# Kernel tuning notes

Hardware: AMD Instinct MI355X
Metric: run time of the kernel (lower is better)

## Reference

```python
import jax, jax.numpy as jnp
import numpy as np

H = 1024          # hidden_size
M = 512           # moe_intermediate_size
E = 16            # num_routed_experts
TOP_K = 2         # num_experts_per_tok
SCALE = 2.5       # routed_scaling_factor
NORM_TOPK = True  # norm_topk_prob
B, S = 1, 1024


def setup_inputs() -> dict:
    key = jax.random.key(0)
    ks = jax.random.split(key, 8)
    std = 0.02
    return {
        "hidden_states": jax.random.normal(ks[0], (B, S, H), jnp.float32),
        "gate_w": jax.random.normal(ks[1], (E, H), jnp.float32) * std,
        "w_gate": jax.random.normal(ks[2], (E, H, M), jnp.float32) * std,
        "w_up": jax.random.normal(ks[3], (E, H, M), jnp.float32) * std,
        "w_down": jax.random.normal(ks[4], (E, M, H), jnp.float32) * std,
        "ws_gate": jax.random.normal(ks[5], (H, M), jnp.float32) * std,
        "ws_up": jax.random.normal(ks[6], (H, M), jnp.float32) * std,
        "ws_down": jax.random.normal(ks[7], (M, H), jnp.float32) * std,
    }


def _moe(x, gate_w, w_gate, w_up, w_down, ws_gate, ws_up, ws_down):
    # x: [T, H] flattened tokens
    T = x.shape[0]
    # shared expert (SwiGLU): down(silu(gate(x)) * up(x))
    shared = (jax.nn.silu(x @ ws_gate) * (x @ ws_up)) @ ws_down  # [T, H]

    # sigmoid gating in fp32 (matches F.linear on fp32 + sigmoid)
    scores = jax.nn.sigmoid(x.astype(jnp.float32) @ gate_w.T.astype(jnp.float32))  # [T, E]
    topk_w, topk_idx = jax.lax.top_k(scores, TOP_K)  # [T, K]
    if NORM_TOPK and TOP_K > 1:
        topk_w = topk_w / (topk_w.sum(-1, keepdims=True) + 1e-20)
    topk_w = topk_w * SCALE

    # dense combine weights [T, E]; zero for non-selected experts, so weighting
    # all-expert outputs is mathematically identical to the dispatch/gather path
    route = jnp.zeros((T, E), topk_w.dtype).at[jnp.arange(T)[:, None], topk_idx].set(topk_w)

    # per-expert SwiGLU over all tokens (grouped-GEMM reference)
    g = jnp.einsum("th,ehm->etm", x, w_gate)                 # [E, T, M]
    u = jnp.einsum("th,ehm->etm", x, w_up)                   # [E, T, M]
    eo = jnp.einsum("etm,emh->eth", jax.nn.silu(g) * u, w_down)  # [E, T, H]
    routed = jnp.einsum("te,eth->th", route.astype(x.dtype), eo)  # [T, H]
    return routed + shared


def reference(hidden_states, gate_w, w_gate, w_up, w_down, ws_gate, ws_up, ws_down):
    b, s, h = hidden_states.shape
    x = hidden_states.reshape(-1, h)
    out = _moe(x, gate_w, w_gate, w_up, w_down, ws_gate, ws_up, ws_down)
    return out.reshape(b, s, h)
```

## Files before the change

### kernel.cpp

```cpp
#include <hip/hip_runtime.h>
#include <math.h>

#define TT 1024
#define HH 1024
#define MM 512
#define NE 16

typedef _Float16 f16;
typedef _Float16 f16x4 __attribute__((ext_vector_type(4)));
typedef _Float16 f16x8 __attribute__((ext_vector_type(8)));
typedef float f32x4 __attribute__((ext_vector_type(4)));

#define GLL(g, l) __builtin_amdgcn_global_load_lds(                         \
    (const __attribute__((address_space(1))) void*)(g),                     \
    (__attribute__((address_space(3))) void*)(l), 16, 0, 0)
#define SB() __builtin_amdgcn_sched_barrier(0)
#define WAITVM(N) { SB(); asm volatile("s_waitcnt vmcnt(" #N ")"); SB(); }
#define BARRIER() __builtin_amdgcn_s_barrier()

__global__ __launch_bounds__(256) void pack_k(const float* __restrict__ x, f16* __restrict__ xh)
{
    const int i = (blockIdx.x * 256 + threadIdx.x) * 4;
    float4 v = *(const float4*)(x + i);
    f16x4 h = { (f16)v.x, (f16)v.y, (f16)v.z, (f16)v.w };
    *(f16x4*)(xh + i) = h;
}

__global__ __launch_bounds__(256) void router_k(
    const float* __restrict__ x, const float* __restrict__ gate_w,
    int* __restrict__ counts, int* __restrict__ token_list, float* __restrict__ weight_list)
{
    const int wave = threadIdx.x >> 6;
    const int lane = threadIdx.x & 63;
    const int t = (blockIdx.x << 2) + wave;
    const float* xr = x + (size_t)t * HH;
    float xv[16];
#pragma unroll
    for (int i = 0; i < 16; ++i) xv[i] = xr[lane + (i << 6)];
    float sc[NE];
#pragma unroll
    for (int e = 0; e < NE; ++e) {
        const float* gr = gate_w + e * HH;
        float acc = 0.f;
#pragma unroll
        for (int i = 0; i < 16; ++i) acc = fmaf(xv[i], gr[lane + (i << 6)], acc);
#pragma unroll
        for (int off = 32; off > 0; off >>= 1) acc += __shfl_down(acc, off, 64);
        sc[e] = acc;
    }
    if (lane == 0) {
        float l1 = -1e30f, l2 = -1e30f; int i1 = 0, i2 = 0;
#pragma unroll
        for (int e = 0; e < NE; ++e) {
            float v = sc[e];
            if (v > l1) { l2 = l1; i2 = i1; l1 = v; i1 = e; }
            else if (v > l2) { l2 = v; i2 = e; }
        }
        float w1 = 1.f / (1.f + __expf(-l1));
        float w2 = 1.f / (1.f + __expf(-l2));
        const float inv = 2.5f / (w1 + w2 + 1e-20f);
        w1 *= inv; w2 *= inv;
        int s1 = atomicAdd(&counts[i1], 1);
        token_list[i1 * TT + s1] = t;
        weight_list[i1 * TT + s1] = w1;
        int s2 = atomicAdd(&counts[i2], 1);
        token_list[i2 * TT + s2] = t;
        weight_list[i2 * TT + s2] = w2;
    }
}

__global__ void prefix_k(const int* __restrict__ counts, int* __restrict__ offs)
{
    if (threadIdx.x == 0 && blockIdx.x == 0) {
        int acc = 0;
#pragma unroll
        for (int e = 0; e < NE; ++e) { offs[e] = acc; acc += counts[e]; }
        offs[NE] = acc;
    }
}


#define GU_ISSUE(T2, AS, BG, BU) {                                          \
    _Pragma("unroll") for (int i = 0; i < 2; ++i) {                         \
        GLL(pA[i] + ((T2) << 6), &AS[(w << 4) + (i << 3)][0]);              \
        GLL(pBg[i] + (size_t)((T2) << 6) * MM, &BG[(w << 4) + (i << 3)][0]);\
        GLL(pBu[i] + (size_t)((T2) << 6) * MM, &BU[(w << 4) + (i << 3)][0]); } }

#define GU_COMP(AS, BG, BU) {                                               \
    _Pragma("unroll") for (int h = 0; h < 2; ++h) {                         \
        const int kb = (h << 5) + (lg << 3);                                \
        const int ko = (h << 2) + lg;                                       \
        f16x8 af[2];                                                        \
        _Pragma("unroll") for (int f = 0; f < 2; ++f) {                     \
            const int m = wm + (f << 4) + lm;                               \
            af[f] = *(const f16x8*)&AS[m][(ko ^ (m & 7)) << 3];             \
        }                                                                   \
        const int bc = (wn + lm) ^ ((lg & 1) << 4);                         \
        f16x8 bg, bu;                                                       \
        _Pragma("unroll") for (int j = 0; j < 8; ++j) {                     \
            bg[j] = (f16)BG[kb + j][bc]; bu[j] = (f16)BU[kb + j][bc]; }     \
        _Pragma("unroll") for (int f = 0; f < 2; ++f) {                     \
            accg[f] = __builtin_amdgcn_mfma_f32_16x16x32_f16(af[f], bg, accg[f], 0, 0, 0); \
            accu[f] = __builtin_amdgcn_mfma_f32_16x16x32_f16(af[f], bu, accu[f], 0, 0, 0); } } }

#define GU_PHI(T2, AI, BC, VC) { GU_ISSUE(T2, As##AI, Bg##AI, Bu##AI)       \
    WAITVM(VC) BARRIER();                                                   \
    GU_COMP(As##BC, Bg##BC, Bu##BC) BARRIER(); }
#define GU_PHN(BC, VC) { WAITVM(VC) BARRIER();                              \
    GU_COMP(As##BC, Bg##BC, Bu##BC) BARRIER(); }

__global__ __launch_bounds__(256) void gu_k(
    const f16* __restrict__ xh,
    const float* __restrict__ w_gate, const float* __restrict__ w_up,
    const float* __restrict__ ws_gate, const float* __restrict__ ws_up,
    const int* __restrict__ counts, const int* __restrict__ offs,
    const int* __restrict__ token_list, f16* __restrict__ rinter)
{
    const int F = blockIdx.x;
    const int Q = F & 7;
    const int J = F >> 3;
    int e, tile;
    if (J < 512) { e = Q + ((J >> 8) << 3); tile = J & 255; }
    else         { e = NE; tile = (Q << 5) + (J - 512); }
    const int n0 = (tile & 15) << 5;
    const int r0 = (tile >> 4) << 6;

    int cnt, slot0;
    const float *wgp, *wup;
    if (e < NE) {
        cnt = counts[e]; slot0 = offs[e];
        wgp = w_gate + (size_t)e * HH * MM;
        wup = w_up   + (size_t)e * HH * MM;
    } else {
        cnt = TT; slot0 = 2 * TT;
        wgp = ws_gate; wup = ws_up;
    }
    if (r0 >= cnt) return;

    __shared__ f16  As0[64][64], As1[64][64], As2[64][64];
    __shared__ float Bg0[64][32], Bg1[64][32], Bg2[64][32];
    __shared__ float Bu0[64][32], Bu1[64][32], Bu2[64][32];
    __shared__ int toks[64];

    const int tid = threadIdx.x;
    if (tid < 64) {
        int i = r0 + tid; if (i >= cnt) i = cnt - 1;
        toks[tid] = (e < NE) ? token_list[e * TT + i] : i;
    }
    __syncthreads();

    const int w = tid >> 6, lane = tid & 63;
    const int lm = lane & 15, lg = lane >> 4;
    const int wm = (w >> 1) << 5, wn = (w & 1) << 4;

    const f16* pA[2];
#pragma unroll
    for (int i = 0; i < 2; ++i) {
        int m = (w << 4) + (i << 3) + (lane >> 3);
        pA[i] = xh + (size_t)toks[m] * HH + (((lane & 7) ^ (lane >> 3)) << 3);
    }
    const float* pBg[2]; const float* pBu[2];
#pragma unroll
    for (int i = 0; i < 2; ++i) {
        int kr = (w << 4) + (i << 3) + (lane >> 3);
        int sg = 4 * ((lane & 7) ^ ((i & 1) << 2));
        pBg[i] = wgp + (size_t)kr * MM + n0 + sg;
        pBu[i] = wup + (size_t)kr * MM + n0 + sg;
    }

    f32x4 accg[2] = {}, accu[2] = {};

    GU_ISSUE(0, As0, Bg0, Bu0)
    GU_ISSUE(1, As1, Bg1, Bu1)

    GU_PHI(2,2,0,12)  GU_PHI(3,0,1,12)  GU_PHI(4,1,2,12)  GU_PHI(5,2,0,12)
    GU_PHI(6,0,1,12)  GU_PHI(7,1,2,12)  GU_PHI(8,2,0,12)  GU_PHI(9,0,1,12)
    GU_PHI(10,1,2,12) GU_PHI(11,2,0,12) GU_PHI(12,0,1,12) GU_PHI(13,1,2,12)
    GU_PHI(14,2,0,12) GU_PHI(15,0,1,12)
    GU_PHN(2,6)       GU_PHN(0,0)

#pragma unroll
    for (int fi = 0; fi < 2; ++fi)
#pragma unroll
        for (int rr = 0; rr < 4; ++rr) {
            const int m = wm + (fi << 4) + (lg << 2) + rr;
            if (r0 + m < cnt) {
                float g = (fi ? accg[1] : accg[0])[rr];
                float u = (fi ? accu[1] : accu[0])[rr];
                float s = g / (1.f + __expf(-g));
                rinter[(size_t)(slot0 + r0 + m) * MM + n0 + wn + lm] = (f16)(s * u);
            }
        }
}


#define DN_ISSUE(T2, AS, BS) {                                              \
    _Pragma("unroll") for (int i = 0; i < 2; ++i) {                         \
        GLL(pa[i] + ((T2) << 6), &AS[(w << 4) + (i << 3)][0]);              \
        GLL(pb[i] + (size_t)((T2) << 6) * HH, &BS[(w << 4) + (i << 3)][0]); } }

#define DN_COMP(AS, BS) {                                                   \
    _Pragma("unroll") for (int h = 0; h < 2; ++h) {                         \
        const int kb = (h << 5) + (lg << 3);                                \
        const int ko = (h << 2) + lg;                                       \
        f16x8 af[2];                                                        \
        _Pragma("unroll") for (int f = 0; f < 2; ++f) {                     \
            const int m = wm + (f << 4) + lm;                               \
            af[f] = *(const f16x8*)&AS[m][(ko ^ (m & 7)) << 3];             \
        }                                                                   \
        const int bc = (wn + lm) ^ ((lg & 1) << 4);                         \
        f16x8 bv;                                                           \
        _Pragma("unroll") for (int j = 0; j < 8; ++j) bv[j] = (f16)BS[kb + j][bc]; \
        _Pragma("unroll") for (int f = 0; f < 2; ++f)                       \
            acc[f] = __builtin_amdgcn_mfma_f32_16x16x32_f16(af[f], bv, acc[f], 0, 0, 0); } }

#define DN_PHI(T2, AI, BC, VC) { DN_ISSUE(T2, As##AI, Bs##AI)               \
    WAITVM(VC) BARRIER();                                                   \
    DN_COMP(As##BC, Bs##BC) BARRIER(); }
#define DN_PHN(BC, VC) { WAITVM(VC) BARRIER();                              \
    DN_COMP(As##BC, Bs##BC) BARRIER(); }

__global__ __launch_bounds__(256) void down_k(
    const f16* __restrict__ rinter,
    const float* __restrict__ w_down, const float* __restrict__ ws_down,
    const int* __restrict__ counts, const int* __restrict__ offs,
    const int* __restrict__ token_list, const float* __restrict__ weight_list,
    float* __restrict__ out)
{
    const int F = blockIdx.x;
    const int Q = F & 7;
    const int J = F >> 3;
    int e, tile;
    if (J < 1024) { e = Q + ((J >> 9) << 3); tile = J & 511; }
    else          { e = NE; tile = (Q << 6) + (J - 1024); }
    const int n0 = (tile & 31) << 5;
    const int r0 = (tile >> 5) << 6;

    int cnt, slot0; const float* wdp;
    if (e < NE) { cnt = counts[e]; slot0 = offs[e]; wdp = w_down + (size_t)e * MM * HH; }
    else        { cnt = TT; slot0 = 2 * TT; wdp = ws_down; }
    if (r0 >= cnt) return;

    __shared__ f16  As0[64][64], As1[64][64], As2[64][64];
    __shared__ float Bs0[64][32], Bs1[64][32], Bs2[64][32];

    const int tid = threadIdx.x;
    const int w = tid >> 6, lane = tid & 63;
    const int lm = lane & 15, lg = lane >> 4;
    const int wm = (w >> 1) << 5, wn = (w & 1) << 4;

    const f16* pa[2];
#pragma unroll
    for (int i = 0; i < 2; ++i) {
        int m = (w << 4) + (i << 3) + (lane >> 3);
        pa[i] = rinter + (size_t)(slot0 + r0 + m) * MM + (((lane & 7) ^ (lane >> 3)) << 3);
    }
    const float* pb[2];
#pragma unroll
    for (int i = 0; i < 2; ++i) {
        int kr = (w << 4) + (i << 3) + (lane >> 3);
        pb[i] = wdp + (size_t)kr * HH + n0 + 4 * ((lane & 7) ^ ((i & 1) << 2));
    }

    f32x4 acc[2] = {};

    DN_ISSUE(0, As0, Bs0)
    DN_ISSUE(1, As1, Bs1)

    DN_PHI(2,2,0,8) DN_PHI(3,0,1,8) DN_PHI(4,1,2,8)
    DN_PHI(5,2,0,8) DN_PHI(6,0,1,8) DN_PHI(7,1,2,8)
    DN_PHN(0,4)     DN_PHN(1,0)

#pragma unroll
    for (int fi = 0; fi < 2; ++fi)
#pragma unroll
        for (int rr = 0; rr < 4; ++rr) {
            const int m = wm + (fi << 4) + (lg << 2) + rr;
            const int row = r0 + m;
            if (row < cnt) {
                int t; float wt;
                if (e < NE) { t = token_list[e * TT + row]; wt = weight_list[e * TT + row]; }
                else        { t = row; wt = 1.f; }
                float v = (fi ? acc[1] : acc[0])[rr];
                atomicAdd(&out[(size_t)t * HH + n0 + wn + lm], wt * v);
            }
        }
}

extern "C" void kernel_launch(void* const* d_in, const int* in_sizes, int n_in,
                              void* d_out, int out_size, void* d_ws, size_t ws_size,
                              hipStream_t stream)
{
    const float* x       = (const float*)d_in[0];
    const float* gate_w  = (const float*)d_in[1];
    const float* w_gate  = (const float*)d_in[2];
    const float* w_up    = (const float*)d_in[3];
    const float* w_down  = (const float*)d_in[4];
    const float* ws_gate = (const float*)d_in[5];
    const float* ws_up   = (const float*)d_in[6];
    const float* ws_down = (const float*)d_in[7];
    float* out = (float*)d_out;

    int* counts = (int*)d_ws;
    int* offs = counts + 16;
    int* token_list = counts + 64;
    float* weight_list = (float*)(counts + 64 + NE * TT);
    f16* rinter = (f16*)(counts + 64 + 2 * NE * TT);
    f16* xh = rinter + (size_t)3072 * MM;

    hipMemsetAsync(counts, 0, 64, stream);
    hipMemsetAsync(out, 0, (size_t)TT * HH * sizeof(float), stream);
    pack_k<<<dim3(TT * HH / 1024), 256, 0, stream>>>(x, xh);
    router_k<<<dim3(TT / 4), 256, 0, stream>>>(x, gate_w, counts, token_list, weight_list);
    prefix_k<<<1, 64, 0, stream>>>(counts, offs);
    gu_k<<<dim3(8 * 544), 256, 0, stream>>>(
        xh, w_gate, w_up, ws_gate, ws_up, counts, offs, token_list, rinter);
    down_k<<<dim3(8 * 1088), 256, 0, stream>>>(
        rinter, w_down, ws_down, counts, offs, token_list, weight_list, out);
}
```

Before: 104.1 us.

## Load A operand directly from global into registers, bypassing LDS staging

Both the gate/up and down GEMM kernels stop staging the fp16 activation tile through shared memory. Each lane now loads its MFMA A fragments straight from global memory into registers, double-buffered one k-step ahead, while the B weights still go through LDS via async loads. This removes the A-tile LDS traffic and frees LDS, at the cost of more uncoalesced global loads, more registers, and vmcnt wait counts that now have to account for the register loads.

New measurement: 133.7 us. 1.28x slower.

```diff
diff --git a/kernel.cpp b/kernel.cpp
--- a/kernel.cpp
+++ b/kernel.cpp
@@ -80,34 +80,36 @@
 }
 
 
-#define GU_ISSUE(T2, AS, BG, BU) {                                          \
+#define GU_ALOAD(S, T1) {                                                   \
+    aa##S##_[0] = *(const f16x8*)(pa0 + ((T1) << 6));                       \
+    aa##S##_[1] = *(const f16x8*)(pa0 + ((T1) << 6) + 32);                  \
+    aa##S##_[2] = *(const f16x8*)(pa1 + ((T1) << 6));                       \
+    aa##S##_[3] = *(const f16x8*)(pa1 + ((T1) << 6) + 32); }
+
+#define GU_BISSUE(T2, BG, BU) {                                             \
     _Pragma("unroll") for (int i = 0; i < 2; ++i) {                         \
-        GLL(pA[i] + ((T2) << 6), &AS[(w << 4) + (i << 3)][0]);              \
         GLL(pBg[i] + (size_t)((T2) << 6) * MM, &BG[(w << 4) + (i << 3)][0]);\
         GLL(pBu[i] + (size_t)((T2) << 6) * MM, &BU[(w << 4) + (i << 3)][0]); } }
 
-#define GU_COMP(AS, BG, BU) {                                               \
+#define GU_COMP(S, BG, BU) {                                                \
     _Pragma("unroll") for (int h = 0; h < 2; ++h) {                         \
         const int kb = (h << 5) + (lg << 3);                                \
-        const int ko = (h << 2) + lg;                                       \
-        f16x8 af[2];                                                        \
-        _Pragma("unroll") for (int f = 0; f < 2; ++f) {                     \
-            const int m = wm + (f << 4) + lm;                               \
-            af[f] = *(const f16x8*)&AS[m][(ko ^ (m & 7)) << 3];             \
-        }                                                                   \
         const int bc = (wn + lm) ^ ((lg & 1) << 4);                         \
         f16x8 bg, bu;                                                       \
         _Pragma("unroll") for (int j = 0; j < 8; ++j) {                     \
             bg[j] = (f16)BG[kb + j][bc]; bu[j] = (f16)BU[kb + j][bc]; }     \
-        _Pragma("unroll") for (int f = 0; f < 2; ++f) {                     \
-            accg[f] = __builtin_amdgcn_mfma_f32_16x16x32_f16(af[f], bg, accg[f], 0, 0, 0); \
-            accu[f] = __builtin_amdgcn_mfma_f32_16x16x32_f16(af[f], bu, accu[f], 0, 0, 0); } } }
-
-#define GU_PHI(T2, AI, BC, VC) { GU_ISSUE(T2, As##AI, Bg##AI, Bu##AI)       \
+        accg[0] = __builtin_amdgcn_mfma_f32_16x16x32_f16(aa##S##_[h],     bg, accg[0], 0, 0, 0); \
+        accg[1] = __builtin_amdgcn_mfma_f32_16x16x32_f16(aa##S##_[2 + h], bg, accg[1], 0, 0, 0); \
+        accu[0] = __builtin_amdgcn_mfma_f32_16x16x32_f16(aa##S##_[h],     bu, accu[0], 0, 0, 0); \
+        accu[1] = __builtin_amdgcn_mfma_f32_16x16x32_f16(aa##S##_[2 + h], bu, accu[1], 0, 0, 0); } }
+
+#define GU_PH(T, SL, SU, BI, BC, VC) {                                      \
+    if ((T) + 1 < 16) GU_ALOAD(SL, (T) + 1)                                 \
+    SB();                                                                   \
+    if ((T) + 2 < 16) GU_BISSUE((T) + 2, Bg##BI, Bu##BI)                    \
     WAITVM(VC) BARRIER();                                                   \
-    GU_COMP(As##BC, Bg##BC, Bu##BC) BARRIER(); }
-#define GU_PHN(BC, VC) { WAITVM(VC) BARRIER();                              \
-    GU_COMP(As##BC, Bg##BC, Bu##BC) BARRIER(); }
+    GU_COMP(SU, Bg##BC, Bu##BC)                                             \
+    BARRIER(); }
 
 __global__ __launch_bounds__(256) void gu_k(
     const f16* __restrict__ xh,
@@ -137,7 +139,6 @@
     }
     if (r0 >= cnt) return;
 
-    __shared__ f16  As0[64][64], As1[64][64], As2[64][64];
     __shared__ float Bg0[64][32], Bg1[64][32], Bg2[64][32];
     __shared__ float Bu0[64][32], Bu1[64][32], Bu2[64][32];
     __shared__ int toks[64];
@@ -153,12 +154,8 @@
     const int lm = lane & 15, lg = lane >> 4;
     const int wm = (w >> 1) << 5, wn = (w & 1) << 4;
 
-    const f16* pA[2];
-#pragma unroll
-    for (int i = 0; i < 2; ++i) {
-        int m = (w << 4) + (i << 3) + (lane >> 3);
-        pA[i] = xh + (size_t)toks[m] * HH + (((lane & 7) ^ (lane >> 3)) << 3);
-    }
+    const f16* pa0 = xh + (size_t)toks[wm + lm]      * HH + (lg << 3);
+    const f16* pa1 = xh + (size_t)toks[wm + 16 + lm] * HH + (lg << 3);
     const float* pBg[2]; const float* pBu[2];
 #pragma unroll
     for (int i = 0; i < 2; ++i) {
@@ -169,15 +166,21 @@
     }
 
     f32x4 accg[2] = {}, accu[2] = {};
-
-    GU_ISSUE(0, As0, Bg0, Bu0)
-    GU_ISSUE(1, As1, Bg1, Bu1)
-
-    GU_PHI(2,2,0,12)  GU_PHI(3,0,1,12)  GU_PHI(4,1,2,12)  GU_PHI(5,2,0,12)
-    GU_PHI(6,0,1,12)  GU_PHI(7,1,2,12)  GU_PHI(8,2,0,12)  GU_PHI(9,0,1,12)
-    GU_PHI(10,1,2,12) GU_PHI(11,2,0,12) GU_PHI(12,0,1,12) GU_PHI(13,1,2,12)
-    GU_PHI(14,2,0,12) GU_PHI(15,0,1,12)
-    GU_PHN(2,6)       GU_PHN(0,0)
+    f16x8 aa0_[4], aa1_[4];
+
+    GU_ALOAD(0, 0)
+    SB();
+    GU_BISSUE(0, Bg0, Bu0)
+    GU_BISSUE(1, Bg1, Bu1)
+
+    GU_PH(0, 1, 0, 2, 0, 12)   GU_PH(1, 0, 1, 0, 1, 12)
+    GU_PH(2, 1, 0, 1, 2, 12)   GU_PH(3, 0, 1, 2, 0, 12)
+    GU_PH(4, 1, 0, 0, 1, 12)   GU_PH(5, 0, 1, 1, 2, 12)
+    GU_PH(6, 1, 0, 2, 0, 12)   GU_PH(7, 0, 1, 0, 1, 12)
+    GU_PH(8, 1, 0, 1, 2, 12)   GU_PH(9, 0, 1, 2, 0, 12)
+    GU_PH(10, 1, 0, 0, 1, 12)  GU_PH(11, 0, 1, 1, 2, 12)
+    GU_PH(12, 1, 0, 2, 0, 12)  GU_PH(13, 0, 1, 0, 1, 12)
+    GU_PH(14, 1, 0, 0, 2, 12)  GU_PH(15, 0, 1, 0, 0, 0)
 
 #pragma unroll
     for (int fi = 0; fi < 2; ++fi)
@@ -194,31 +197,32 @@
 }
 
 
-#define DN_ISSUE(T2, AS, BS) {                                              \
-    _Pragma("unroll") for (int i = 0; i < 2; ++i) {                         \
-        GLL(pa[i] + ((T2) << 6), &AS[(w << 4) + (i << 3)][0]);              \
-        GLL(pb[i] + (size_t)((T2) << 6) * HH, &BS[(w << 4) + (i << 3)][0]); } }
-
-#define DN_COMP(AS, BS) {                                                   \
+#define DN_ALOAD(S, T1) {                                                   \
+    ad##S##_[0] = *(const f16x8*)(pa0 + ((T1) << 6));                       \
+    ad##S##_[1] = *(const f16x8*)(pa0 + ((T1) << 6) + 32);                  \
+    ad##S##_[2] = *(const f16x8*)(pa1 + ((T1) << 6));                       \
+    ad##S##_[3] = *(const f16x8*)(pa1 + ((T1) << 6) + 32); }
+
+#define DN_BISSUE(T2, BS) {                                                 \
+    _Pragma("unroll") for (int i = 0; i < 2; ++i)                           \
+        GLL(pb[i] + (size_t)((T2) << 6) * HH, &BS[(w << 4) + (i << 3)][0]); }
+
+#define DN_COMP(S, BS) {                                                    \
     _Pragma("unroll") for (int h = 0; h < 2; ++h) {                         \
         const int kb = (h << 5) + (lg << 3);                                \
-        const int ko = (h << 2) + lg;                                       \
-        f16x8 af[2];                                                        \
-        _Pragma("unroll") for (int f = 0; f < 2; ++f) {                     \
-            const int m = wm + (f << 4) + lm;                               \
-            af[f] = *(const f16x8*)&AS[m][(ko ^ (m & 7)) << 3];             \
-        }                                                                   \
         const int bc = (wn + lm) ^ ((lg & 1) << 4);                         \
         f16x8 bv;                                                           \
         _Pragma("unroll") for (int j = 0; j < 8; ++j) bv[j] = (f16)BS[kb + j][bc]; \
-        _Pragma("unroll") for (int f = 0; f < 2; ++f)                       \
-            acc[f] = __builtin_amdgcn_mfma_f32_16x16x32_f16(af[f], bv, acc[f], 0, 0, 0); } }
-
-#define DN_PHI(T2, AI, BC, VC) { DN_ISSUE(T2, As##AI, Bs##AI)               \
+        acc[0] = __builtin_amdgcn_mfma_f32_16x16x32_f16(ad##S##_[h],     bv, acc[0], 0, 0, 0); \
+        acc[1] = __builtin_amdgcn_mfma_f32_16x16x32_f16(ad##S##_[2 + h], bv, acc[1], 0, 0, 0); } }
+
+#define DN_PH(T, SL, SU, BI, BC, VC) {                                      \
+    if ((T) + 1 < 8) DN_ALOAD(SL, (T) + 1)                                  \
+    SB();                                                                   \
+    if ((T) + 2 < 8) DN_BISSUE((T) + 2, Bs##BI)                             \
     WAITVM(VC) BARRIER();                                                   \
-    DN_COMP(As##BC, Bs##BC) BARRIER(); }
-#define DN_PHN(BC, VC) { WAITVM(VC) BARRIER();                              \
-    DN_COMP(As##BC, Bs##BC) BARRIER(); }
+    DN_COMP(SU, Bs##BC)                                                     \
+    BARRIER(); }
 
 __global__ __launch_bounds__(256) void down_k(
     const f16* __restrict__ rinter,
@@ -241,7 +245,6 @@
     else        { cnt = TT; slot0 = 2 * TT; wdp = ws_down; }
     if (r0 >= cnt) return;
 
-    __shared__ f16  As0[64][64], As1[64][64], As2[64][64];
     __shared__ float Bs0[64][32], Bs1[64][32], Bs2[64][32];
 
     const int tid = threadIdx.x;
@@ -249,12 +252,8 @@
     const int lm = lane & 15, lg = lane >> 4;
     const int wm = (w >> 1) << 5, wn = (w & 1) << 4;
 
-    const f16* pa[2];
-#pragma unroll
-    for (int i = 0; i < 2; ++i) {
-        int m = (w << 4) + (i << 3) + (lane >> 3);
-        pa[i] = rinter + (size_t)(slot0 + r0 + m) * MM + (((lane & 7) ^ (lane >> 3)) << 3);
-    }
+    const f16* pa0 = rinter + (size_t)(slot0 + r0 + wm + lm)      * MM + (lg << 3);
+    const f16* pa1 = rinter + (size_t)(slot0 + r0 + wm + 16 + lm) * MM + (lg << 3);
     const float* pb[2];
 #pragma unroll
     for (int i = 0; i < 2; ++i) {
@@ -263,13 +262,17 @@
     }
 
     f32x4 acc[2] = {};
-
-    DN_ISSUE(0, As0, Bs0)
-    DN_ISSUE(1, As1, Bs1)
-
-    DN_PHI(2,2,0,8) DN_PHI(3,0,1,8) DN_PHI(4,1,2,8)
-    DN_PHI(5,2,0,8) DN_PHI(6,0,1,8) DN_PHI(7,1,2,8)
-    DN_PHN(0,4)     DN_PHN(1,0)
+    f16x8 ad0_[4], ad1_[4];
+
+    DN_ALOAD(0, 0)
+    SB();
+    DN_BISSUE(0, Bs0)
+    DN_BISSUE(1, Bs1)
+
+    DN_PH(0, 1, 0, 2, 0, 8)   DN_PH(1, 0, 1, 0, 1, 12)
+    DN_PH(2, 1, 0, 1, 2, 12)  DN_PH(3, 0, 1, 2, 0, 12)
+    DN_PH(4, 1, 0, 0, 1, 12)  DN_PH(5, 0, 1, 1, 2, 12)
+    DN_PH(6, 1, 0, 0, 0, 8)   DN_PH(7, 0, 1, 0, 1, 0)
 
 #pragma unroll
     for (int fi = 0; fi < 2; ++fi)
```

## Retile gate/up GEMM to 128-row tiles with 512 threads and 4-stage pipeline

Applied to the files above, without the earlier changes.

The gate/up grouped GEMM kernel now uses 128-token tiles with 8 waves per block (512 threads) instead of 64-token tiles with 4 waves. The K step per stage shrinks from 64 to 32, and the ring of shared-memory buffers grows from three to four, with three stages issued ahead. Each weight tile is now reused across twice as many tokens, which cuts repeated fp32 weight traffic per expert. The cost is more padding waste for experts with small token counts and fewer, larger blocks in the grid. The loop is no longer unrolled, which adds a little loop overhead.

Result: no change. 105.8 us (+1.6%).

```diff
diff --git a/kernel.cpp b/kernel.cpp
--- a/kernel.cpp
+++ b/kernel.cpp
@@ -80,36 +80,34 @@
 }
 
 
-#define GU_ISSUE(T2, AS, BG, BU) {                                          \
-    _Pragma("unroll") for (int i = 0; i < 2; ++i) {                         \
-        GLL(pA[i] + ((T2) << 6), &AS[(w << 4) + (i << 3)][0]);              \
-        GLL(pBg[i] + (size_t)((T2) << 6) * MM, &BG[(w << 4) + (i << 3)][0]);\
-        GLL(pBu[i] + (size_t)((T2) << 6) * MM, &BU[(w << 4) + (i << 3)][0]); } }
+#define GU_ISSUE(KT, AS, BG, BU) {                                          \
+    GLL(pA + (size_t)((KT) << 5), &AS[w << 4][0]);                          \
+    GLL(pB + (size_t)((KT) << 5) * MM, (w < 4) ? &BG[(w & 3) << 3][0]       \
+                                               : &BU[(w & 3) << 3][0]); }
 
 #define GU_COMP(AS, BG, BU) {                                               \
-    _Pragma("unroll") for (int h = 0; h < 2; ++h) {                         \
-        const int kb = (h << 5) + (lg << 3);                                \
-        const int ko = (h << 2) + lg;                                       \
-        f16x8 af[2];                                                        \
-        _Pragma("unroll") for (int f = 0; f < 2; ++f) {                     \
-            const int m = wm + (f << 4) + lm;                               \
-            af[f] = *(const f16x8*)&AS[m][(ko ^ (m & 7)) << 3];             \
-        }                                                                   \
-        const int bc = (wn + lm) ^ ((lg & 1) << 4);                         \
-        f16x8 bg, bu;                                                       \
-        _Pragma("unroll") for (int j = 0; j < 8; ++j) {                     \
-            bg[j] = (f16)BG[kb + j][bc]; bu[j] = (f16)BU[kb + j][bc]; }     \
-        _Pragma("unroll") for (int f = 0; f < 2; ++f) {                     \
-            accg[f] = __builtin_amdgcn_mfma_f32_16x16x32_f16(af[f], bg, accg[f], 0, 0, 0); \
-            accu[f] = __builtin_amdgcn_mfma_f32_16x16x32_f16(af[f], bu, accu[f], 0, 0, 0); } } }
-
-#define GU_PHI(T2, AI, BC, VC) { GU_ISSUE(T2, As##AI, Bg##AI, Bu##AI)       \
+    f16x8 af[2];                                                            \
+    _Pragma("unroll") for (int f = 0; f < 2; ++f) {                         \
+        const int m = wm + (f << 4) + lm;                                   \
+        af[f] = *(const f16x8*)&AS[m][(lg ^ (m & 3)) << 3];                 \
+    }                                                                       \
+    const int bc = (wn + lm) ^ ((lg & 1) << 4);                             \
+    f16x8 bg, bu;                                                           \
+    _Pragma("unroll") for (int j = 0; j < 8; ++j) {                         \
+        bg[j] = (f16)BG[(lg << 3) + j][bc];                                 \
+        bu[j] = (f16)BU[(lg << 3) + j][bc]; }                               \
+    accg[0] = __builtin_amdgcn_mfma_f32_16x16x32_f16(af[0], bg, accg[0], 0, 0, 0); \
+    accg[1] = __builtin_amdgcn_mfma_f32_16x16x32_f16(af[1], bg, accg[1], 0, 0, 0); \
+    accu[0] = __builtin_amdgcn_mfma_f32_16x16x32_f16(af[0], bu, accu[0], 0, 0, 0); \
+    accu[1] = __builtin_amdgcn_mfma_f32_16x16x32_f16(af[1], bu, accu[1], 0, 0, 0); }
+
+#define GU_PH(KT, IB, CB, VC) {                                             \
+    if ((KT) + 3 < 32) GU_ISSUE((KT) + 3, As##IB, Bg##IB, Bu##IB)           \
     WAITVM(VC) BARRIER();                                                   \
-    GU_COMP(As##BC, Bg##BC, Bu##BC) BARRIER(); }
-#define GU_PHN(BC, VC) { WAITVM(VC) BARRIER();                              \
-    GU_COMP(As##BC, Bg##BC, Bu##BC) BARRIER(); }
-
-__global__ __launch_bounds__(256) void gu_k(
+    GU_COMP(As##CB, Bg##CB, Bu##CB)                                         \
+    BARRIER(); }
+
+__global__ __launch_bounds__(512) void gu_k(
     const f16* __restrict__ xh,
     const float* __restrict__ w_gate, const float* __restrict__ w_up,
     const float* __restrict__ ws_gate, const float* __restrict__ ws_up,
@@ -119,11 +117,17 @@
     const int F = blockIdx.x;
     const int Q = F & 7;
     const int J = F >> 3;
-    int e, tile;
-    if (J < 512) { e = Q + ((J >> 8) << 3); tile = J & 255; }
-    else         { e = NE; tile = (Q << 5) + (J - 512); }
-    const int n0 = (tile & 15) << 5;
-    const int r0 = (tile >> 4) << 6;
+    int e, n0, r0;
+    if (J < 256) {
+        e = Q + ((J >> 7) << 3);
+        n0 = (J & 15) << 5;
+        r0 = ((J & 127) >> 4) << 7;
+    } else {
+        e = NE;
+        int idx = (Q << 4) + (J - 256);
+        n0 = (idx & 15) << 5;
+        r0 = (idx >> 4) << 7;
+    }
 
     int cnt, slot0;
     const float *wgp, *wup;
@@ -137,13 +141,13 @@
     }
     if (r0 >= cnt) return;
 
-    __shared__ f16  As0[64][64], As1[64][64], As2[64][64];
-    __shared__ float Bg0[64][32], Bg1[64][32], Bg2[64][32];
-    __shared__ float Bu0[64][32], Bu1[64][32], Bu2[64][32];
-    __shared__ int toks[64];
+    __shared__ f16  As0[128][32], As1[128][32], As2[128][32], As3[128][32];
+    __shared__ float Bg0[32][32], Bg1[32][32], Bg2[32][32], Bg3[32][32];
+    __shared__ float Bu0[32][32], Bu1[32][32], Bu2[32][32], Bu3[32][32];
+    __shared__ int toks[128];
 
     const int tid = threadIdx.x;
-    if (tid < 64) {
+    if (tid < 128) {
         int i = r0 + tid; if (i >= cnt) i = cnt - 1;
         toks[tid] = (e < NE) ? token_list[e * TT + i] : i;
     }
@@ -151,33 +155,33 @@
 
     const int w = tid >> 6, lane = tid & 63;
     const int lm = lane & 15, lg = lane >> 4;
-    const int wm = (w >> 1) << 5, wn = (w & 1) << 4;
-
-    const f16* pA[2];
-#pragma unroll
-    for (int i = 0; i < 2; ++i) {
-        int m = (w << 4) + (i << 3) + (lane >> 3);
-        pA[i] = xh + (size_t)toks[m] * HH + (((lane & 7) ^ (lane >> 3)) << 3);
-    }
-    const float* pBg[2]; const float* pBu[2];
-#pragma unroll
-    for (int i = 0; i < 2; ++i) {
-        int kr = (w << 4) + (i << 3) + (lane >> 3);
-        int sg = 4 * ((lane & 7) ^ ((i & 1) << 2));
-        pBg[i] = wgp + (size_t)kr * MM + n0 + sg;
-        pBu[i] = wup + (size_t)kr * MM + n0 + sg;
-    }
+    const int wm = (w >> 1) << 5;
+    const int wn = (w & 1) << 4;
+
+    const int arow = (w << 4) + (lane >> 2);
+    const f16* pA = xh + (size_t)toks[arow] * HH
+                       + (size_t)(((lane & 3) ^ ((lane >> 2) & 3)) << 3);
+    const int kr = ((w & 3) << 3) + (lane >> 3);
+    const int sg = 4 * ((lane & 7) ^ ((w & 1) << 2));
+    const float* pB = ((w < 4) ? wgp : wup) + (size_t)kr * MM + n0 + sg;
 
     f32x4 accg[2] = {}, accu[2] = {};
 
     GU_ISSUE(0, As0, Bg0, Bu0)
     GU_ISSUE(1, As1, Bg1, Bu1)
-
-    GU_PHI(2,2,0,12)  GU_PHI(3,0,1,12)  GU_PHI(4,1,2,12)  GU_PHI(5,2,0,12)
-    GU_PHI(6,0,1,12)  GU_PHI(7,1,2,12)  GU_PHI(8,2,0,12)  GU_PHI(9,0,1,12)
-    GU_PHI(10,1,2,12) GU_PHI(11,2,0,12) GU_PHI(12,0,1,12) GU_PHI(13,1,2,12)
-    GU_PHI(14,2,0,12) GU_PHI(15,0,1,12)
-    GU_PHN(2,6)       GU_PHN(0,0)
+    GU_ISSUE(2, As2, Bg2, Bu2)
+
+#pragma unroll 1
+    for (int kt = 0; kt < 28; kt += 4) {
+        GU_PH(kt + 0, 3, 0, 6)
+        GU_PH(kt + 1, 0, 1, 6)
+        GU_PH(kt + 2, 1, 2, 6)
+        GU_PH(kt + 3, 2, 3, 6)
+    }
+    GU_PH(28, 3, 0, 6)
+    { WAITVM(4) BARRIER(); GU_COMP(As1, Bg1, Bu1) BARRIER(); }
+    { WAITVM(2) BARRIER(); GU_COMP(As2, Bg2, Bu2) BARRIER(); }
+    { WAITVM(0) BARRIER(); GU_COMP(As3, Bg3, Bu3) BARRIER(); }
 
 #pragma unroll
     for (int fi = 0; fi < 2; ++fi)
@@ -313,7 +317,7 @@
     pack_k<<<dim3(TT * HH / 1024), 256, 0, stream>>>(x, xh);
     router_k<<<dim3(TT / 4), 256, 0, stream>>>(x, gate_w, counts, token_list, weight_list);
     prefix_k<<<1, 64, 0, stream>>>(counts, offs);
-    gu_k<<<dim3(8 * 544), 256, 0, stream>>>(
+    gu_k<<<dim3(8 * 272), 512, 0, stream>>>(
         xh, w_gate, w_up, ws_gate, ws_up, counts, offs, token_list, rinter);
     down_k<<<dim3(8 * 1088), 256, 0, stream>>>(
         rinter, w_down, ws_down, counts, offs, token_list, weight_list, out);
```

## Enlarge down-projection tiles to 128x64 with 32-wide K steps

Applied to the files above, without the earlier changes.

The down kernel's output tile grows from 64x32 to 128x64, with K stepped in chunks of 32 over 16 triple-buffered phases. Each wave now computes 32 rows by 64 columns, reusing its A fragments across four B column fragments. This cuts redundant global loads of w_down and rinter and divides the block count by four. In exchange, each block holds more accumulator registers, the grid is coarser so load balance for small experts may suffer, and out-of-range rows are clamped to avoid reads past the end.

New measurement: 99.83 us. 4.1% less time.

```diff
diff --git a/kernel.cpp b/kernel.cpp
--- a/kernel.cpp
+++ b/kernel.cpp
@@ -194,31 +194,30 @@
 }
 
 
-#define DN_ISSUE(T2, AS, BS) {                                              \
-    _Pragma("unroll") for (int i = 0; i < 2; ++i) {                         \
-        GLL(pa[i] + ((T2) << 6), &AS[(w << 4) + (i << 3)][0]);              \
-        GLL(pb[i] + (size_t)((T2) << 6) * HH, &BS[(w << 4) + (i << 3)][0]); } }
+#define DN_ISSUE(T, AS, BS) {                                               \
+    GLL(pa0 + ((T) << 5), &AS[w << 5][0]);                                  \
+    GLL(pa1 + ((T) << 5), &AS[(w << 5) + 16][0]);                           \
+    GLL(pb0 + (size_t)((T) << 5) * HH, &BS[w << 3][0]);                     \
+    GLL(pb1 + (size_t)((T) << 5) * HH, &BS[(w << 3) + 4][0]); }
 
 #define DN_COMP(AS, BS) {                                                   \
-    _Pragma("unroll") for (int h = 0; h < 2; ++h) {                         \
-        const int kb = (h << 5) + (lg << 3);                                \
-        const int ko = (h << 2) + lg;                                       \
-        f16x8 af[2];                                                        \
-        _Pragma("unroll") for (int f = 0; f < 2; ++f) {                     \
-            const int m = wm + (f << 4) + lm;                               \
-            af[f] = *(const f16x8*)&AS[m][(ko ^ (m & 7)) << 3];             \
-        }                                                                   \
-        const int bc = (wn + lm) ^ ((lg & 1) << 4);                         \
+    f16x8 af[2];                                                            \
+    _Pragma("unroll") for (int f = 0; f < 2; ++f) {                         \
+        const int m = (w << 5) + (f << 4) + lm;                             \
+        af[f] = *(const f16x8*)&AS[m][(lg ^ ((m >> 1) & 3)) << 3];          \
+    }                                                                       \
+    _Pragma("unroll") for (int nf = 0; nf < 4; ++nf) {                      \
+        const int bc = ((nf << 4) + lm) ^ ((lg & 1) << 4);                  \
         f16x8 bv;                                                           \
-        _Pragma("unroll") for (int j = 0; j < 8; ++j) bv[j] = (f16)BS[kb + j][bc]; \
+        _Pragma("unroll") for (int j = 0; j < 8; ++j) bv[j] = (f16)BS[(lg << 3) + j][bc]; \
         _Pragma("unroll") for (int f = 0; f < 2; ++f)                       \
-            acc[f] = __builtin_amdgcn_mfma_f32_16x16x32_f16(af[f], bv, acc[f], 0, 0, 0); } }
-
-#define DN_PHI(T2, AI, BC, VC) { DN_ISSUE(T2, As##AI, Bs##AI)               \
+            acc[f][nf] = __builtin_amdgcn_mfma_f32_16x16x32_f16(af[f], bv, acc[f][nf], 0, 0, 0); } }
+
+#define DN_PH(T, CB, IB, VC) {                                              \
+    if ((T) + 2 < 16) DN_ISSUE((T) + 2, As##IB, Bs##IB)                     \
     WAITVM(VC) BARRIER();                                                   \
-    DN_COMP(As##BC, Bs##BC) BARRIER(); }
-#define DN_PHN(BC, VC) { WAITVM(VC) BARRIER();                              \
-    DN_COMP(As##BC, Bs##BC) BARRIER(); }
+    DN_COMP(As##CB, Bs##CB)                                                 \
+    BARRIER(); }
 
 __global__ __launch_bounds__(256) void down_k(
     const f16* __restrict__ rinter,
@@ -230,59 +229,64 @@
     const int F = blockIdx.x;
     const int Q = F & 7;
     const int J = F >> 3;
-    int e, tile;
-    if (J < 1024) { e = Q + ((J >> 9) << 3); tile = J & 511; }
-    else          { e = NE; tile = (Q << 6) + (J - 1024); }
-    const int n0 = (tile & 31) << 5;
-    const int r0 = (tile >> 5) << 6;
+    int e, n0, r0;
+    if (J < 256) {
+        e = Q + ((J >> 7) << 3);
+        const int t = J & 127;
+        n0 = (t & 15) << 6;
+        r0 = (t >> 4) << 7;
+    } else {
+        e = NE;
+        const int idx = (Q << 4) + (J - 256);
+        n0 = (idx & 15) << 6;
+        r0 = (idx >> 4) << 7;
+    }
 
     int cnt, slot0; const float* wdp;
     if (e < NE) { cnt = counts[e]; slot0 = offs[e]; wdp = w_down + (size_t)e * MM * HH; }
     else        { cnt = TT; slot0 = 2 * TT; wdp = ws_down; }
     if (r0 >= cnt) return;
 
-    __shared__ f16  As0[64][64], As1[64][64], As2[64][64];
-    __shared__ float Bs0[64][32], Bs1[64][32], Bs2[64][32];
+    __shared__ f16  As0[128][32], As1[128][32], As2[128][32];
+    __shared__ float Bs0[32][64], Bs1[32][64], Bs2[32][64];
 
     const int tid = threadIdx.x;
     const int w = tid >> 6, lane = tid & 63;
     const int lm = lane & 15, lg = lane >> 4;
-    const int wm = (w >> 1) << 5, wn = (w & 1) << 4;
-
-    const f16* pa[2];
-#pragma unroll
-    for (int i = 0; i < 2; ++i) {
-        int m = (w << 4) + (i << 3) + (lane >> 3);
-        pa[i] = rinter + (size_t)(slot0 + r0 + m) * MM + (((lane & 7) ^ (lane >> 3)) << 3);
-    }
-    const float* pb[2];
-#pragma unroll
-    for (int i = 0; i < 2; ++i) {
-        int kr = (w << 4) + (i << 3) + (lane >> 3);
-        pb[i] = wdp + (size_t)kr * HH + n0 + 4 * ((lane & 7) ^ ((i & 1) << 2));
-    }
-
-    f32x4 acc[2] = {};
+
+    const int swzA = ((lane & 3) ^ ((lane >> 3) & 3)) << 3;
+    int ra = r0 + (w << 5) + (lane >> 2);       if (ra >= cnt) ra = cnt - 1;
+    int rb = r0 + (w << 5) + 16 + (lane >> 2);  if (rb >= cnt) rb = cnt - 1;
+    const f16* pa0 = rinter + (size_t)(slot0 + ra) * MM + swzA;
+    const f16* pa1 = rinter + (size_t)(slot0 + rb) * MM + swzA;
+    const int sgd = 4 * ((lane & 15) ^ ((w & 1) << 2));
+    const float* pb0 = wdp + (size_t)((w << 3)     + (lane >> 4)) * HH + n0 + sgd;
+    const float* pb1 = wdp + (size_t)((w << 3) + 4 + (lane >> 4)) * HH + n0 + sgd;
+
+    f32x4 acc[2][4] = {};
 
     DN_ISSUE(0, As0, Bs0)
     DN_ISSUE(1, As1, Bs1)
 
-    DN_PHI(2,2,0,8) DN_PHI(3,0,1,8) DN_PHI(4,1,2,8)
-    DN_PHI(5,2,0,8) DN_PHI(6,0,1,8) DN_PHI(7,1,2,8)
-    DN_PHN(0,4)     DN_PHN(1,0)
-
-#pragma unroll
-    for (int fi = 0; fi < 2; ++fi)
+    DN_PH(0,0,2,8)  DN_PH(1,1,0,8)  DN_PH(2,2,1,8)  DN_PH(3,0,2,8)
+    DN_PH(4,1,0,8)  DN_PH(5,2,1,8)  DN_PH(6,0,2,8)  DN_PH(7,1,0,8)
+    DN_PH(8,2,1,8)  DN_PH(9,0,2,8)  DN_PH(10,1,0,8) DN_PH(11,2,1,8)
+    DN_PH(12,0,2,8) DN_PH(13,1,0,8) DN_PH(14,2,1,4) DN_PH(15,0,0,0)
+
+#pragma unroll
+    for (int f = 0; f < 2; ++f)
 #pragma unroll
         for (int rr = 0; rr < 4; ++rr) {
-            const int m = wm + (fi << 4) + (lg << 2) + rr;
+            const int m = (w << 5) + (f << 4) + (lg << 2) + rr;
             const int row = r0 + m;
             if (row < cnt) {
                 int t; float wt;
                 if (e < NE) { t = token_list[e * TT + row]; wt = weight_list[e * TT + row]; }
                 else        { t = row; wt = 1.f; }
-                float v = (fi ? acc[1] : acc[0])[rr];
-                atomicAdd(&out[(size_t)t * HH + n0 + wn + lm], wt * v);
+                float* orow = out + (size_t)t * HH + n0;
+#pragma unroll
+                for (int nf = 0; nf < 4; ++nf)
+                    atomicAdd(&orow[(nf << 4) + lm], wt * acc[f][nf][rr]);
             }
         }
 }
@@ -315,6 +319,6 @@
     prefix_k<<<1, 64, 0, stream>>>(counts, offs);
     gu_k<<<dim3(8 * 544), 256, 0, stream>>>(
         xh, w_gate, w_up, ws_gate, ws_up, counts, offs, token_list, rinter);
-    down_k<<<dim3(8 * 1088), 256, 0, stream>>>(
+    down_k<<<dim3(8 * 272), 256, 0, stream>>>(
         rinter, w_down, ws_down, counts, offs, token_list, weight_list, out);
 }
```
